# Optimization experiments

Hardware: AMD Instinct MI355X
Metric: run time of the kernel (lower is better)

Reference implementation:

```python
import jax, jax.numpy as jnp
import numpy as np

B, S, H, E, D, K = 2, 4096, 1024, 8, 2048, 2


def setup_inputs() -> dict:
    key = jax.random.key(0)
    ks = jax.random.split(key, 6)
    scale = 0.02
    return {
        "x": jax.random.normal(ks[0], (B, S, H), dtype=jnp.float32),
        "gate_w": jax.random.normal(ks[1], (E, H), dtype=jnp.float32) * scale,
        "w1": jax.random.normal(ks[2], (E, H, D), dtype=jnp.float32) * scale,
        "b1": jnp.zeros((E, D), dtype=jnp.float32),
        "w2": jax.random.normal(ks[3], (E, D, H), dtype=jnp.float32) * scale,
        "b2": jnp.zeros((E, H), dtype=jnp.float32),
    }


def reference(x, gate_w, w1, b1, w2, b2):
    b, s, h = x.shape
    e = gate_w.shape[0]
    # Router
    router_logits = jnp.einsum('bsh,eh->bse', x, gate_w)
    router_probs = jax.nn.softmax(router_logits, axis=-1)
    top_k_probs, expert_idx = jax.lax.top_k(router_probs, K)      # [B,S,K]
    top_k_probs = top_k_probs / top_k_probs.sum(axis=-1, keepdims=True)
    # Aux load-balancing loss (faithful to source: mean over batch only -> [S,E])
    oh = jax.nn.one_hot(expert_idx, e, dtype=x.dtype)             # [B,S,K,E]
    tokens_per_expert = oh.sum(axis=-2).mean(axis=0)              # [S,E]
    avg_prob = router_probs.mean(axis=(0, 1))                     # [E]
    aux_loss = e * (tokens_per_expert * avg_prob).sum()
    # Dense combine weights per token per expert: [B*S, E]
    combine = (oh * top_k_probs[..., None]).sum(axis=-2).reshape(-1, e)
    # Expert MLPs, batched over experts (grouped GEMM form)
    xf = x.reshape(-1, h)                                         # [T,H]
    hid = jax.nn.gelu(jnp.einsum('th,ehd->etd', xf, w1) + b1[:, None, :],
                      approximate=False)                          # [E,T,D]
    y = jnp.einsum('etd,edh->eth', hid, w2) + b2[:, None, :]      # [E,T,H]
    out = jnp.einsum('te,eth->th', combine, y)                    # [T,H]
    return out.reshape(b, s, h), aux_loss
```

## Files before the change

kernel.cpp:

```cpp
#include <hip/hip_runtime.h>
#include <hip/hip_bf16.h>
#include <math.h>

#define Bdim 2
#define Sdim 4096
#define Hdim 1024
#define Edim 8
#define Ddim 2048
#define Tdim (Bdim*Sdim)

typedef __attribute__((ext_vector_type(8))) __bf16 bfv8;
typedef __attribute__((ext_vector_type(8))) short s16x8;
typedef __attribute__((ext_vector_type(4))) short s16x4;
typedef __attribute__((ext_vector_type(4))) float f32x4;

__device__ __forceinline__ short f2bf(float f) {
    union { float f; unsigned u; } a; a.f = f;
    unsigned r = (a.u + 0x7fffu + ((a.u >> 16) & 1u)) >> 16;
    return (short)r;
}
__device__ __forceinline__ float bf2f(short s) {
    union { unsigned u; float f; } a; a.u = ((unsigned)(unsigned short)s) << 16;
    return a.f;
}
__device__ __forceinline__ float fgelu(float x) {
    float u = fminf(x * (1.5957691f + 0.07135481f * x * x), 60.0f);
    float t = __expf(u);
    return x * t / (t + 1.0f);
}

typedef const __attribute__((address_space(1))) unsigned int ga_u32;
typedef __attribute__((address_space(3))) unsigned int la_u32;

__device__ __forceinline__ void gl_lds16(const void* g, void* l) {
    __builtin_amdgcn_global_load_lds((ga_u32*)g, (la_u32*)l, 16, 0, 0);
}

#define WAIT_BAR(N) do {                                     \
    asm volatile("s_waitcnt vmcnt(" #N ")" ::: "memory");    \
    __builtin_amdgcn_s_barrier();                            \
    __builtin_amdgcn_sched_barrier(0);                       \
} while (0)

__global__ __launch_bounds__(256) void router_kernel(
    const float* __restrict__ x, const float* __restrict__ gw,
    int* __restrict__ cnt, float* __restrict__ psum,
    int* __restrict__ ltok, float* __restrict__ lw,
    short* __restrict__ xb)
{
    __shared__ float gws[Edim * Hdim];
    __shared__ int   lcnt[Edim], gbase[Edim];
    __shared__ int   s_e[32], s_pos[32], s_tok[32];
    __shared__ float s_w[32];
    __shared__ float s_ps[4][8];

    int tid = threadIdx.x;
    for (int i = tid; i < Edim * Hdim / 4; i += 256)
        ((float4*)gws)[i] = ((const float4*)gw)[i];
    if (tid < Edim) lcnt[tid] = 0;
    __syncthreads();

    int wave = tid >> 6, lane = tid & 63;
    float ps = 0.f;

    for (int i = 0; i < 4; ++i) {
        int t = blockIdx.x * 16 + wave * 4 + i;
        double acc[Edim];
#pragma unroll
        for (int e = 0; e < Edim; ++e) acc[e] = 0.0;
#pragma unroll
        for (int kq = 0; kq < 4; ++kq) {
            float4 xv = *(const float4*)(x + (size_t)t * Hdim + kq * 256 + lane * 4);
            if (xb) {
                s16x4 h; h[0]=f2bf(xv.x); h[1]=f2bf(xv.y); h[2]=f2bf(xv.z); h[3]=f2bf(xv.w);
                *(s16x4*)(xb + (size_t)t * Hdim + kq * 256 + lane * 4) = h;
            }
#pragma unroll
            for (int e = 0; e < Edim; ++e) {
                float4 wv = *(const float4*)(&gws[e * Hdim + kq * 256 + lane * 4]);
                acc[e] += (double)xv.x * wv.x + (double)xv.y * wv.y
                        + (double)xv.z * wv.z + (double)xv.w * wv.w;
            }
        }
#pragma unroll
        for (int e = 0; e < Edim; ++e) {
            acc[e] += __shfl_xor(acc[e], 1, 64);
            acc[e] += __shfl_xor(acc[e], 2, 64);
            acc[e] += __shfl_xor(acc[e], 4, 64);
        }
        int el = lane & 7;
        double v = acc[0];
#pragma unroll
        for (int e = 1; e < Edim; ++e) if (el == e) v = acc[e];
        v += __shfl_xor(v, 8, 64);
        v += __shfl_xor(v, 16, 64);
// ... 42 lines not shown
        int pos = gbase[e] + s_pos[tid];
        ltok[e * Tdim + pos] = s_tok[tid];
        lw[e * Tdim + pos] = s_w[tid];
    }
}

__global__ void aux_kernel(const int* __restrict__ cnt,
                           const float* __restrict__ psum,
                           int* __restrict__ eoff,
                           float* __restrict__ out_aux)
{
    if (threadIdx.x == 0 && blockIdx.x == 0) {
        double s = 0.0;
        int run = 0;
        for (int e = 0; e < Edim; ++e) {
            eoff[e] = run;
            run += cnt[e];
            s += ((double)cnt[e] / (double)Bdim) * ((double)psum[e] / (double)Tdim);
        }
        out_aux[0] = (float)((double)Edim * s);
    }
}

__global__ __launch_bounds__(256) void convt_kernel(const float* __restrict__ w,
                                                    short* __restrict__ wt, int R, int C)
{
    int e = blockIdx.z;
    int r0 = blockIdx.y * 64, c0 = blockIdx.x * 64;
    __shared__ short t[64][76];
    int tid = threadIdx.x;
    {
        int r = tid >> 2, cs = (tid & 3) * 16;
        const float* src = w + ((size_t)e * R + r0 + r) * C + c0 + cs;
#pragma unroll
        for (int q = 0; q < 4; ++q) {
            float4 v = *(const float4*)(src + q * 4);
            s16x4 h; h[0]=f2bf(v.x); h[1]=f2bf(v.y); h[2]=f2bf(v.z); h[3]=f2bf(v.w);
            *(s16x4*)(&t[r][cs + q * 4]) = h;
        }
    }
    __syncthreads();
    {
        int c = tid >> 2, rs = (tid & 3) * 16;
        short tmp[16];
#pragma unroll
        for (int j = 0; j < 16; ++j) tmp[j] = t[rs + j][c];
        short* dst = wt + ((size_t)e * C + c0 + c) * R + r0 + rs;
        *(s16x8*)dst = *(s16x8*)tmp;
        *(s16x8*)(dst + 8) = *(s16x8*)(tmp + 8);
    }
}


__global__ __launch_bounds__(512, 2) void gemm1n_kernel(
    const short* __restrict__ xb, const short* __restrict__ w1t,
    const float* __restrict__ b1, const int* __restrict__ cnt,
    const int* __restrict__ eoff, const int* __restrict__ ltok,
    short* __restrict__ hid)
{
    constexpr int GXN = Ddim / 256;
    int id = blockIdx.x;
    int e = id & 7;
    unsigned rem = (unsigned)id >> 3;
    int bx = rem & (GXN - 1);
    int by = rem / GXN;

    int n_e = cnt[e];
    int row0 = by * 256;
    if (row0 >= n_e) return;
    int col0 = bx * 256;
    int slot0 = eoff[e];

    __shared__ short lds[65536];
    char* ldsb = (char*)lds;

    int tid = threadIdx.x;
    int w = tid >> 6, lane = tid & 63;

    const short* aS[2]; const short* bS[2];
    int oA[2];
#pragma unroll
    for (int j = 0; j < 2; ++j) {
        int o = tid * 16 + j * 8192;
        oA[j] = o;
        int eff = o ^ (((o >> 7) & 7) << 4);
        int row = ((eff >> 7) << 1) | ((eff >> 6) & 1);
        int kB  = eff & 63;
        int gr = row0 + row; if (gr > n_e - 1) gr = n_e - 1;
        int tok = ltok[(size_t)e * Tdim + gr] >> 1;
        aS[j] = xb + (size_t)tok * Hdim + (kB >> 1);
        bS[j] = w1t + ((size_t)e * Ddim + col0 + row) * Hdim + (kB >> 1);
    }

    int fr = lane & 15, kg = lane >> 4;
    int wm = (w >> 2) * 128, wn = (w & 3) * 64;

    int offA[8], offB[4];
#pragma unroll
    for (int m = 0; m < 8; ++m) {
        int r = wm + m * 16 + fr;
        offA[m] = (r >> 1) * 64 + ((((r & 1) * 32) + kg * 8) ^ (((r >> 1) & 7) << 3));
    }
#pragma unroll
    for (int n = 0; n < 4; ++n) {
        int r = wn + n * 16 + fr;
        offB[n] = (r >> 1) * 64 + ((((r & 1) * 32) + kg * 8) ^ (((r >> 1) & 7) << 3));
    }

    f32x4 acc[8][4];
#pragma unroll
    for (int m = 0; m < 8; ++m)
#pragma unroll
        for (int n = 0; n < 4; ++n) acc[m][n] = (f32x4)0.0f;

    auto stage = [&](int dstB) {
#pragma unroll
        for (int j = 0; j < 2; ++j) {
            gl_lds16(aS[j], ldsb + dstB + oA[j]);
            gl_lds16(bS[j], ldsb + dstB + 32768 + oA[j]);
            aS[j] += 32; bS[j] += 32;
        }
    };
    auto computeH = [&](int baseSh) {
        bfv8 af[8], bf[4];
#pragma unroll
        for (int n = 0; n < 4; ++n) bf[n] = *(const bfv8*)(lds + baseSh + 16384 + offB[n]);
#pragma unroll
        for (int m = 0; m < 8; ++m) af[m] = *(const bfv8*)(lds + baseSh + offA[m]);
        __builtin_amdgcn_s_setprio(1);
#pragma unroll
        for (int m = 0; m < 8; ++m)
#pragma unroll
            for (int n = 0; n < 4; ++n)
                acc[m][n] = __builtin_amdgcn_mfma_f32_16x16x32_bf16(af[m], bf[n], acc[m][n], 0, 0, 0);
        __builtin_amdgcn_s_setprio(0);
    };

    constexpr int NK = Hdim / 64;
    stage(0);
    stage(16384);
    for (int k = 0; k < NK - 2; k += 2) {
        stage(65536);         WAIT_BAR(8); computeH(0);
        stage(65536 + 16384); WAIT_BAR(8); computeH(8192);
        stage(0);             WAIT_BAR(8); computeH(32768);
        stage(16384);         WAIT_BAR(8); computeH(40960);
    }
    stage(65536);         WAIT_BAR(8); computeH(0);
    stage(65536 + 16384); WAIT_BAR(8); computeH(8192);
    WAIT_BAR(4); computeH(32768);
    WAIT_BAR(0); computeH(40960);

#pragma unroll
    for (int m = 0; m < 8; ++m) {
        int r0r = wm + m * 16 + kg * 4;
#pragma unroll
        for (int j = 0; j < 4; ++j) {
            int gr = row0 + r0r + j;
            if (gr >= n_e) continue;
            size_t hbase = (size_t)(slot0 + gr) * Ddim;
#pragma unroll
            for (int n = 0; n < 4; ++n) {
                int col = col0 + wn + n * 16 + fr;
                float v = acc[m][n][j] + b1[e * Ddim + col];
                hid[hbase + col] = f2bf(fgelu(v));
            }
        }
    }
}

__global__ __launch_bounds__(512, 2) void gemm2n_kernel(
    const short* __restrict__ hid, const short* __restrict__ w2t,
    const float* __restrict__ b2, const int* __restrict__ cnt,
    const int* __restrict__ eoff, const int* __restrict__ ltok,
    const float* __restrict__ lw, short* __restrict__ out2)
{
    constexpr int GXN = Hdim / 256;
    int id = blockIdx.x;
    int e = id & 7;
    unsigned rem = (unsigned)id >> 3;
    int bx = rem & (GXN - 1);
    int by = rem / GXN;

    int n_e = cnt[e];
    int row0 = by * 256;
    if (row0 >= n_e) return;
    int col0 = bx * 256;
    int slot0 = eoff[e];

    __shared__ short lds[65536];
    char* ldsb = (char*)lds;

    int tid = threadIdx.x;
    int w = tid >> 6, lane = tid & 63;

    const short* aS[2]; const short* bS[2];
    int oA[2];
#pragma unroll
    for (int j = 0; j < 2; ++j) {
        int o = tid * 16 + j * 8192;
        oA[j] = o;
        int eff = o ^ (((o >> 7) & 7) << 4);
        int row = ((eff >> 7) << 1) | ((eff >> 6) & 1);
        int kB  = eff & 63;
        int gr = row0 + row; if (gr > n_e - 1) gr = n_e - 1;
        aS[j] = hid + (size_t)(slot0 + gr) * Ddim + (kB >> 1);
        bS[j] = w2t + ((size_t)e * Hdim + col0 + row) * Ddim + (kB >> 1);
    }

    int fr = lane & 15, kg = lane >> 4;
    int wm = (w >> 2) * 128, wn = (w & 3) * 64;

    int offA[8], offB[4];
#pragma unroll
    for (int m = 0; m < 8; ++m) {
        int r = wm + m * 16 + fr;
        offA[m] = (r >> 1) * 64 + ((((r & 1) * 32) + kg * 8) ^ (((r >> 1) & 7) << 3));
    }
#pragma unroll
    for (int n = 0; n < 4; ++n) {
        int r = wn + n * 16 + fr;
        offB[n] = (r >> 1) * 64 + ((((r & 1) * 32) + kg * 8) ^ (((r >> 1) & 7) << 3));
    }

    f32x4 acc[8][4];
#pragma unroll
    for (int m = 0; m < 8; ++m)
#pragma unroll
        for (int n = 0; n < 4; ++n) acc[m][n] = (f32x4)0.0f;

    auto stage = [&](int dstB) {
#pragma unroll
        for (int j = 0; j < 2; ++j) {
            gl_lds16(aS[j], ldsb + dstB + oA[j]);
            gl_lds16(bS[j], ldsb + dstB + 32768 + oA[j]);
            aS[j] += 32; bS[j] += 32;
        }
    };
    auto computeH = [&](int baseSh) {
        bfv8 af[8], bf[4];
#pragma unroll
        for (int n = 0; n < 4; ++n) bf[n] = *(const bfv8*)(lds + baseSh + 16384 + offB[n]);
#pragma unroll
        for (int m = 0; m < 8; ++m) af[m] = *(const bfv8*)(lds + baseSh + offA[m]);
        __builtin_amdgcn_s_setprio(1);
#pragma unroll
        for (int m = 0; m < 8; ++m)
#pragma unroll
            for (int n = 0; n < 4; ++n)
                acc[m][n] = __builtin_amdgcn_mfma_f32_16x16x32_bf16(af[m], bf[n], acc[m][n], 0, 0, 0);
        __builtin_amdgcn_s_setprio(0);
    };

    constexpr int NK = Ddim / 64;
    stage(0);
    stage(16384);
    for (int k = 0; k < NK - 2; k += 2) {
        stage(65536);         WAIT_BAR(8); computeH(0);
        stage(65536 + 16384); WAIT_BAR(8); computeH(8192);
        stage(0);             WAIT_BAR(8); computeH(32768);
        stage(16384);         WAIT_BAR(8); computeH(40960);
    }
    stage(65536);         WAIT_BAR(8); computeH(0);
    stage(65536 + 16384); WAIT_BAR(8); computeH(8192);
    WAIT_BAR(4); computeH(32768);
    WAIT_BAR(0); computeH(40960);

#pragma unroll
    for (int m = 0; m < 8; ++m) {
        int r0r = wm + m * 16 + kg * 4;
#pragma unroll
        for (int j = 0; j < 4; ++j) {
            int gr = row0 + r0r + j;
            if (gr >= n_e) continue;
            int val = ltok[(size_t)e * Tdim + gr];
            float p = lw[(size_t)e * Tdim + gr];
            size_t obase = (size_t)val * Hdim;
#pragma unroll
            for (int n = 0; n < 4; ++n) {
                int col = col0 + wn + n * 16 + fr;
                float v = p * (acc[m][n][j] + b2[e * Hdim + col]);
                out2[obase + col] = f2bf(v);
            }
        }
    }
}

__global__ __launch_bounds__(256) void combine_kernel(const short* __restrict__ out2,
                                                      float* __restrict__ out)
{
    size_t i = ((size_t)blockIdx.x * 256 + threadIdx.x) * 8;
    size_t t = i >> 10;
    int h = (int)(i & 1023);
    s16x8 a = *(const s16x8*)(out2 + (t * 2) * 1024 + h);
    s16x8 b = *(const s16x8*)(out2 + (t * 2 + 1) * 1024 + h);
#pragma unroll
    for (int j = 0; j < 8; ++j)
        out[i + j] = bf2f(a[j]) + bf2f(b[j]);
}

#define FBK 64
#define FLDK 72

__global__ __launch_bounds__(256) void gemm1_fb(
    const float* __restrict__ x, const float* __restrict__ w1,
    const float* __restrict__ b1, const int* __restrict__ cnt,
    const int* __restrict__ ltok, short* __restrict__ hid,
    int CH, int row_base)
{
    int e = blockIdx.z;
    int n_e = cnt[e];
    int row0 = row_base + blockIdx.y * 128;
    if (row0 >= n_e) return;
    int col0 = blockIdx.x * 128;

    __shared__ short As[128][FLDK];
    __shared__ short Bs[128][FLDK];

    int tid = threadIdx.x;
    int arow = tid >> 1;
    int akh  = (tid & 1) * 32;
    int gr_a = row0 + arow;
    int tok = ltok[(size_t)e * Tdim + (gr_a < n_e ? gr_a : n_e - 1)] >> 1;
    const float* xrow = x + (size_t)tok * Hdim + akh;
    int bdg = (tid & 31) * 4;
    int bkg = (tid >> 5) * 4;

    int lane = tid & 63;
    int wid = tid >> 6;
    int wm = (wid >> 1) * 64, wn = (wid & 1) * 64;
    int fr = lane & 15, kg = lane >> 4;

    f32x4 acc[4][4];
#pragma unroll
    for (int m = 0; m < 4; ++m)
#pragma unroll
        for (int n = 0; n < 4; ++n) acc[m][n] = (f32x4)0.0f;

    const float* wB = w1 + (size_t)e * Hdim * Ddim + col0;

    for (int k0 = 0; k0 < Hdim; k0 += FBK) {
#pragma unroll
        for (int i = 0; i < 8; ++i) {
            float4 v = *(const float4*)(xrow + k0 + i * 4);
            s16x4 h; h[0] = f2bf(v.x); h[1] = f2bf(v.y); h[2] = f2bf(v.z); h[3] = f2bf(v.w);
            *(s16x4*)(&As[arow][akh + i * 4]) = h;
        }
#pragma unroll
        for (int r = 0; r < 2; ++r) {
            int kq = bkg + r * 32;
            float4 v0 = *(const float4*)(wB + (size_t)(k0 + kq + 0) * Ddim + bdg);
// ... 137 lines not shown
            if (gr >= n_e) continue;
            int tok = ltok[(size_t)e * Tdim + gr] >> 1;
            float p = lw[(size_t)e * Tdim + gr];
#pragma unroll
            for (int n = 0; n < 4; ++n) {
                int col = col0 + wn + n * 16 + fr;
                float v = p * (acc[m][n][j] + b2[e * Hdim + col]);
                atomicAdd(&out[(size_t)tok * Hdim + col], v);
            }
        }
    }
}

extern "C" void kernel_launch(void* const* d_in, const int* in_sizes, int n_in,
                              void* d_out, int out_size, void* d_ws, size_t ws_size,
                              hipStream_t stream)
{
    const float* x  = (const float*)d_in[0];
    const float* gw = (const float*)d_in[1];
    const float* w1 = (const float*)d_in[2];
    const float* b1 = (const float*)d_in[3];
    const float* w2 = (const float*)d_in[4];
    const float* b2 = (const float*)d_in[5];
    float* out = (float*)d_out;

    char* wsb = (char*)d_ws;
    int*   cnt  = (int*)wsb;
    float* psum = (float*)(wsb + 32);
    int*   eoff = (int*)(wsb + 64);
    int*   ltok = (int*)(wsb + 128);
    float* lwp  = (float*)(wsb + 128 + (size_t)Edim * Tdim * 4);
    size_t lists_end = 128 + (size_t)Edim * Tdim * 8;

    size_t xb_sz = (size_t)Tdim * Hdim * 2;
    size_t w1t_sz = (size_t)Edim * Hdim * Ddim * 2;
    size_t w2t_sz = w1t_sz;
    size_t hid_sz = (size_t)(2 * Tdim) * Ddim * 2;
    size_t req = lists_end + xb_sz + w1t_sz + w2t_sz + hid_sz;

    hipMemsetAsync(wsb, 0, 128, stream);

    if (req <= ws_size) {
        short* xb   = (short*)(wsb + lists_end);
        short* w1t  = (short*)(wsb + lists_end + xb_sz);
        short* w2t  = (short*)(wsb + lists_end + xb_sz + w1t_sz);
        short* hid  = (short*)(wsb + lists_end + xb_sz + w1t_sz + w2t_sz);
        short* out2 = w1t;

        convt_kernel<<<dim3(Ddim / 64, Hdim / 64, Edim), 256, 0, stream>>>(w1, w1t, Hdim, Ddim);
        convt_kernel<<<dim3(Hdim / 64, Ddim / 64, Edim), 256, 0, stream>>>(w2, w2t, Ddim, Hdim);
        router_kernel<<<Tdim / 16, 256, 0, stream>>>(x, gw, cnt, psum, ltok, lwp, xb);
        aux_kernel<<<1, 64, 0, stream>>>(cnt, psum, eoff, out + (size_t)Tdim * Hdim);

        gemm1n_kernel<<<(Ddim / 256) * 32 * Edim, 512, 0, stream>>>(
            xb, w1t, b1, cnt, eoff, ltok, hid);
        gemm2n_kernel<<<(Hdim / 256) * 32 * Edim, 512, 0, stream>>>(
            hid, w2t, b2, cnt, eoff, ltok, lwp, out2);
        combine_kernel<<<(size_t)Tdim * Hdim / 2048, 256, 0, stream>>>(out2, out);
    } else {
        short* hid = (short*)(wsb + lists_end);
        int CH2 = 2048;
        while (CH2 > 128 && lists_end + (size_t)Edim * CH2 * Ddim * 2 > ws_size) CH2 >>= 1;

        hipMemsetAsync(d_out, 0, (size_t)out_size * 4, stream);
        router_kernel<<<Tdim / 16, 256, 0, stream>>>(x, gw, cnt, psum, ltok, lwp, nullptr);
        aux_kernel<<<1, 64, 0, stream>>>(cnt, psum, eoff, out + (size_t)Tdim * Hdim);

        int chunks = Tdim / CH2;
        for (int c = 0; c < chunks; ++c) {
            gemm1_fb<<<dim3(Ddim / 128, CH2 / 128, Edim), 256, 0, stream>>>(
                x, w1, b1, cnt, ltok, hid, CH2, c * CH2);
            gemm2_fb<<<dim3(Hdim / 128, CH2 / 128, Edim), 256, 0, stream>>>(
                hid, w2, b2, cnt, ltok, lwp, out, CH2, c * CH2);
        }
    }
}
```

Baseline: 337.7 us.

## Retile expert GEMMs to 256x128 with four-stage LDS ring and register double buffering

Both grouped expert GEMMs move from 512-thread 256x256 tiles to 256-thread 256x128 tiles with a K step of 32. LDS becomes a four-slot ring, and the LDS-to-register fragment reads are double buffered so the next slice's reads overlap the current MFMAs. The combine kernel now writes float4 vectors instead of scalar stores. In exchange, the grid doubles, occupancy drops to one block per CU, and there are more barriers per unit of K work.

```diff
diff --git a/kernel.cpp b/kernel.cpp
--- a/kernel.cpp
+++ b/kernel.cpp
@@ -36,10 +36,26 @@
     __builtin_amdgcn_global_load_lds((ga_u32*)g, (la_u32*)l, 16, 0, 0);
 }
 
-#define WAIT_BAR(N) do {                                     \
-    asm volatile("s_waitcnt vmcnt(" #N ")" ::: "memory");    \
-    __builtin_amdgcn_s_barrier();                            \
-    __builtin_amdgcn_sched_barrier(0);                       \
+#define WB(N) do {                                                        \
+    asm volatile("s_waitcnt vmcnt(" #N ") lgkmcnt(0)" ::: "memory");      \
+    __builtin_amdgcn_s_barrier();                                         \
+    __builtin_amdgcn_sched_barrier(0);                                    \
+} while (0)
+
+#define RD(FA, FB, R) do {                                                            \
+    _Pragma("unroll") for (int n = 0; n < 4; ++n)                                     \
+        FB[n] = *(const bfv8*)(lds + 32768 + (R) * 4096 + offB[n]);                   \
+    _Pragma("unroll") for (int m = 0; m < 8; ++m)                                     \
+        FA[m] = *(const bfv8*)(lds + (R) * 8192 + offA[m]);                           \
+    __builtin_amdgcn_sched_barrier(0);                                                \
+} while (0)
+
+#define MM(FA, FB) do {                                                               \
+    __builtin_amdgcn_s_setprio(1);                                                    \
+    _Pragma("unroll") for (int m = 0; m < 8; ++m)                                     \
+        _Pragma("unroll") for (int n = 0; n < 4; ++n)                                 \
+            acc[m][n] = __builtin_amdgcn_mfma_f32_16x16x32_bf16(FA[m], FB[n], acc[m][n], 0, 0, 0); \
+    __builtin_amdgcn_s_setprio(0);                                                    \
 } while (0)
 
 __global__ __launch_bounds__(256) void router_kernel(
@@ -189,13 +205,13 @@
 }
 
 
-__global__ __launch_bounds__(512, 2) void gemm1n_kernel(
+__global__ __launch_bounds__(256, 1) void gemm1n_kernel(
     const short* __restrict__ xb, const short* __restrict__ w1t,
     const float* __restrict__ b1, const int* __restrict__ cnt,
     const int* __restrict__ eoff, const int* __restrict__ ltok,
     short* __restrict__ hid)
 {
-    constexpr int GXN = Ddim / 256;
+    constexpr int GXN = Ddim / 128;
     int id = blockIdx.x;
     int e = id & 7;
     unsigned rem = (unsigned)id >> 3;
@@ -205,32 +221,40 @@
     int n_e = cnt[e];
     int row0 = by * 256;
     if (row0 >= n_e) return;
-    int col0 = bx * 256;
+    int col0 = bx * 128;
     int slot0 = eoff[e];
 
-    __shared__ short lds[65536];
+    __shared__ short lds[49152];
     char* ldsb = (char*)lds;
 
     int tid = threadIdx.x;
     int w = tid >> 6, lane = tid & 63;
 
-    const short* aS[2]; const short* bS[2];
-    int oA[2];
-#pragma unroll
-    for (int j = 0; j < 2; ++j) {
-        int o = tid * 16 + j * 8192;
-        oA[j] = o;
+    const short* aS[4]; const short* bS[2];
+    int oAd[4], oBd[2];
+#pragma unroll
+    for (int j = 0; j < 4; ++j) {
+        int o = tid * 16 + j * 4096;
+        oAd[j] = o;
         int eff = o ^ (((o >> 7) & 7) << 4);
         int row = ((eff >> 7) << 1) | ((eff >> 6) & 1);
         int kB  = eff & 63;
         int gr = row0 + row; if (gr > n_e - 1) gr = n_e - 1;
         int tok = ltok[(size_t)e * Tdim + gr] >> 1;
         aS[j] = xb + (size_t)tok * Hdim + (kB >> 1);
+    }
+#pragma unroll
+    for (int j = 0; j < 2; ++j) {
+        int o = tid * 16 + j * 4096;
+        oBd[j] = o;
+        int eff = o ^ (((o >> 7) & 7) << 4);
+        int row = ((eff >> 7) << 1) | ((eff >> 6) & 1);
+        int kB  = eff & 63;
         bS[j] = w1t + ((size_t)e * Ddim + col0 + row) * Hdim + (kB >> 1);
     }
 
     int fr = lane & 15, kg = lane >> 4;
-    int wm = (w >> 2) * 128, wn = (w & 3) * 64;
+    int wm = (w >> 1) * 128, wn = (w & 1) * 64;
 
     int offA[8], offB[4];
 #pragma unroll
@@ -250,42 +274,35 @@
 #pragma unroll
         for (int n = 0; n < 4; ++n) acc[m][n] = (f32x4)0.0f;
 
-    auto stage = [&](int dstB) {
+    bfv8 f0A[8], f0B[4], f1A[8], f1B[4];
+
+    auto stage = [&](int r) {
+#pragma unroll
+        for (int j = 0; j < 4; ++j) {
+            gl_lds16(aS[j], ldsb + r * 16384 + oAd[j]);
+            aS[j] += 32;
+        }
 #pragma unroll
         for (int j = 0; j < 2; ++j) {
-            gl_lds16(aS[j], ldsb + dstB + oA[j]);
-            gl_lds16(bS[j], ldsb + dstB + 32768 + oA[j]);
-            aS[j] += 32; bS[j] += 32;
+            gl_lds16(bS[j], ldsb + 65536 + r * 8192 + oBd[j]);
+            bS[j] += 32;
         }
     };
-    auto computeH = [&](int baseSh) {
-        bfv8 af[8], bf[4];
-#pragma unroll
-        for (int n = 0; n < 4; ++n) bf[n] = *(const bfv8*)(lds + baseSh + 16384 + offB[n]);
-#pragma unroll
-        for (int m = 0; m < 8; ++m) af[m] = *(const bfv8*)(lds + baseSh + offA[m]);
-        __builtin_amdgcn_s_setprio(1);
-#pragma unroll
-        for (int m = 0; m < 8; ++m)
-#pragma unroll
-            for (int n = 0; n < 4; ++n)
-                acc[m][n] = __builtin_amdgcn_mfma_f32_16x16x32_bf16(af[m], bf[n], acc[m][n], 0, 0, 0);
-        __builtin_amdgcn_s_setprio(0);
-    };
-
-    constexpr int NK = Hdim / 64;
-    stage(0);
-    stage(16384);
-    for (int k = 0; k < NK - 2; k += 2) {
-        stage(65536);         WAIT_BAR(8); computeH(0);
-        stage(65536 + 16384); WAIT_BAR(8); computeH(8192);
-        stage(0);             WAIT_BAR(8); computeH(32768);
-        stage(16384);         WAIT_BAR(8); computeH(40960);
-    }
-    stage(65536);         WAIT_BAR(8); computeH(0);
-    stage(65536 + 16384); WAIT_BAR(8); computeH(8192);
-    WAIT_BAR(4); computeH(32768);
-    WAIT_BAR(0); computeH(40960);
+
+    constexpr int NH = Hdim / 32;
+    stage(0); stage(1);
+    stage(2); WB(12); RD(f0A, f0B, 0);
+    stage(3); WB(12); RD(f1A, f1B, 1); MM(f0A, f0B);
+#pragma unroll 1
+    for (int it = 0; it < (NH - 4) / 4; ++it) {
+        stage(0); WB(12); RD(f0A, f0B, 2); MM(f1A, f1B);
+        stage(1); WB(12); RD(f1A, f1B, 3); MM(f0A, f0B);
+        stage(2); WB(12); RD(f0A, f0B, 0); MM(f1A, f1B);
+        stage(3); WB(12); RD(f1A, f1B, 1); MM(f0A, f0B);
+    }
+    WB(6);  RD(f0A, f0B, 2); MM(f1A, f1B);
+    WB(0);  RD(f1A, f1B, 3); MM(f0A, f0B);
+    MM(f1A, f1B);
 
 #pragma unroll
     for (int m = 0; m < 8; ++m) {
@@ -305,13 +322,13 @@
     }
 }
 
-__global__ __launch_bounds__(512, 2) void gemm2n_kernel(
+__global__ __launch_bounds__(256, 1) void gemm2n_kernel(
     const short* __restrict__ hid, const short* __restrict__ w2t,
     const float* __restrict__ b2, const int* __restrict__ cnt,
     const int* __restrict__ eoff, const int* __restrict__ ltok,
     const float* __restrict__ lw, short* __restrict__ out2)
 {
-    constexpr int GXN = Hdim / 256;
+    constexpr int GXN = Hdim / 128;
     int id = blockIdx.x;
     int e = id & 7;
     unsigned rem = (unsigned)id >> 3;
@@ -321,31 +338,39 @@
     int n_e = cnt[e];
     int row0 = by * 256;
     if (row0 >= n_e) return;
-    int col0 = bx * 256;
+    int col0 = bx * 128;
     int slot0 = eoff[e];
 
-    __shared__ short lds[65536];
+    __shared__ short lds[49152];
     char* ldsb = (char*)lds;
 
     int tid = threadIdx.x;
     int w = tid >> 6, lane = tid & 63;
 
-    const short* aS[2]; const short* bS[2];
-    int oA[2];
-#pragma unroll
-    for (int j = 0; j < 2; ++j) {
-        int o = tid * 16 + j * 8192;
-        oA[j] = o;
+    const short* aS[4]; const short* bS[2];
+    int oAd[4], oBd[2];
+#pragma unroll
+    for (int j = 0; j < 4; ++j) {
+        int o = tid * 16 + j * 4096;
+        oAd[j] = o;
         int eff = o ^ (((o >> 7) & 7) << 4);
         int row = ((eff >> 7) << 1) | ((eff >> 6) & 1);
         int kB  = eff & 63;
         int gr = row0 + row; if (gr > n_e - 1) gr = n_e - 1;
         aS[j] = hid + (size_t)(slot0 + gr) * Ddim + (kB >> 1);
+    }
+#pragma unroll
+    for (int j = 0; j < 2; ++j) {
+        int o = tid * 16 + j * 4096;
+        oBd[j] = o;
+        int eff = o ^ (((o >> 7) & 7) << 4);
+        int row = ((eff >> 7) << 1) | ((eff >> 6) & 1);
+        int kB  = eff & 63;
         bS[j] = w2t + ((size_t)e * Hdim + col0 + row) * Ddim + (kB >> 1);
     }
 
     int fr = lane & 15, kg = lane >> 4;
-    int wm = (w >> 2) * 128, wn = (w & 3) * 64;
+    int wm = (w >> 1) * 128, wn = (w & 1) * 64;
 
     int offA[8], offB[4];
 #pragma unroll
@@ -365,42 +390,35 @@
 #pragma unroll
         for (int n = 0; n < 4; ++n) acc[m][n] = (f32x4)0.0f;
 
-    auto stage = [&](int dstB) {
+    bfv8 f0A[8], f0B[4], f1A[8], f1B[4];
+
+    auto stage = [&](int r) {
+#pragma unroll
+        for (int j = 0; j < 4; ++j) {
+            gl_lds16(aS[j], ldsb + r * 16384 + oAd[j]);
+            aS[j] += 32;
+        }
 #pragma unroll
         for (int j = 0; j < 2; ++j) {
-            gl_lds16(aS[j], ldsb + dstB + oA[j]);
-            gl_lds16(bS[j], ldsb + dstB + 32768 + oA[j]);
-            aS[j] += 32; bS[j] += 32;
+            gl_lds16(bS[j], ldsb + 65536 + r * 8192 + oBd[j]);
+            bS[j] += 32;
         }
     };
-    auto computeH = [&](int baseSh) {
-        bfv8 af[8], bf[4];
-#pragma unroll
-        for (int n = 0; n < 4; ++n) bf[n] = *(const bfv8*)(lds + baseSh + 16384 + offB[n]);
-#pragma unroll
-        for (int m = 0; m < 8; ++m) af[m] = *(const bfv8*)(lds + baseSh + offA[m]);
-        __builtin_amdgcn_s_setprio(1);
-#pragma unroll
-        for (int m = 0; m < 8; ++m)
-#pragma unroll
-            for (int n = 0; n < 4; ++n)
-                acc[m][n] = __builtin_amdgcn_mfma_f32_16x16x32_bf16(af[m], bf[n], acc[m][n], 0, 0, 0);
-        __builtin_amdgcn_s_setprio(0);
-    };
-
-    constexpr int NK = Ddim / 64;
-    stage(0);
-    stage(16384);
-    for (int k = 0; k < NK - 2; k += 2) {
-        stage(65536);         WAIT_BAR(8); computeH(0);
-        stage(65536 + 16384); WAIT_BAR(8); computeH(8192);
-        stage(0);             WAIT_BAR(8); computeH(32768);
-        stage(16384);         WAIT_BAR(8); computeH(40960);
-    }
-    stage(65536);         WAIT_BAR(8); computeH(0);
-    stage(65536 + 16384); WAIT_BAR(8); computeH(8192);
-    WAIT_BAR(4); computeH(32768);
-    WAIT_BAR(0); computeH(40960);
+
+    constexpr int NH = Ddim / 32;
+    stage(0); stage(1);
+    stage(2); WB(12); RD(f0A, f0B, 0);
+    stage(3); WB(12); RD(f1A, f1B, 1); MM(f0A, f0B);
+#pragma unroll 1
+    for (int it = 0; it < (NH - 4) / 4; ++it) {
+        stage(0); WB(12); RD(f0A, f0B, 2); MM(f1A, f1B);
+        stage(1); WB(12); RD(f1A, f1B, 3); MM(f0A, f0B);
+        stage(2); WB(12); RD(f0A, f0B, 0); MM(f1A, f1B);
+        stage(3); WB(12); RD(f1A, f1B, 1); MM(f0A, f0B);
+    }
+    WB(6);  RD(f0A, f0B, 2); MM(f1A, f1B);
+    WB(0);  RD(f1A, f1B, 3); MM(f0A, f0B);
+    MM(f1A, f1B);
 
 #pragma unroll
     for (int m = 0; m < 8; ++m) {
@@ -430,9 +448,13 @@
     int h = (int)(i & 1023);
     s16x8 a = *(const s16x8*)(out2 + (t * 2) * 1024 + h);
     s16x8 b = *(const s16x8*)(out2 + (t * 2 + 1) * 1024 + h);
-#pragma unroll
-    for (int j = 0; j < 8; ++j)
-        out[i + j] = bf2f(a[j]) + bf2f(b[j]);
+    float4 o0, o1;
+    o0.x = bf2f(a[0]) + bf2f(b[0]); o0.y = bf2f(a[1]) + bf2f(b[1]);
+    o0.z = bf2f(a[2]) + bf2f(b[2]); o0.w = bf2f(a[3]) + bf2f(b[3]);
+    o1.x = bf2f(a[4]) + bf2f(b[4]); o1.y = bf2f(a[5]) + bf2f(b[5]);
+    o1.z = bf2f(a[6]) + bf2f(b[6]); o1.w = bf2f(a[7]) + bf2f(b[7]);
+    *(float4*)(out + i) = o0;
+    *(float4*)(out + i + 4) = o1;
 }
 
 #define FBK 64
@@ -676,9 +698,9 @@
         router_kernel<<<Tdim / 16, 256, 0, stream>>>(x, gw, cnt, psum, ltok, lwp, xb);
         aux_kernel<<<1, 64, 0, stream>>>(cnt, psum, eoff, out + (size_t)Tdim * Hdim);
 
-        gemm1n_kernel<<<(Ddim / 256) * 32 * Edim, 512, 0, stream>>>(
+        gemm1n_kernel<<<(Ddim / 128) * 32 * Edim, 256, 0, stream>>>(
             xb, w1t, b1, cnt, eoff, ltok, hid);
-        gemm2n_kernel<<<(Hdim / 256) * 32 * Edim, 512, 0, stream>>>(
+        gemm2n_kernel<<<(Hdim / 128) * 32 * Edim, 256, 0, stream>>>(
             hid, w2t, b2, cnt, eoff, ltok, lwp, out2);
         combine_kernel<<<(size_t)Tdim * Hdim / 2048, 256, 0, stream>>>(out2, out);
     } else {
```

Result: slower. 365.7 us (+8.3%).

## Restructure expert GEMM mainloop into 4-slot pipeline with early LDS reads

Applied to the files above, without the earlier changes.

Both expert GEMM kernels move from a two-half-tile compute per 64-wide K step to a four-slot ring of 32-wide K chunks. A and B now sit in separate LDS halves. Each phase reads fragments from LDS before issuing the next global-to-LDS stage, then waits and runs MFMAs, so LDS reads overlap the in-flight global loads and the per-phase vmcnt waits become looser. The combine kernel now writes float4 vectors instead of scalar stores. The cost is more barriers per K, since there is one per 32-wide chunk, plus tighter ordering via sched_barrier.

```diff
diff --git a/kernel.cpp b/kernel.cpp
--- a/kernel.cpp
+++ b/kernel.cpp
@@ -36,10 +36,43 @@
     __builtin_amdgcn_global_load_lds((ga_u32*)g, (la_u32*)l, 16, 0, 0);
 }
 
-#define WAIT_BAR(N) do {                                     \
-    asm volatile("s_waitcnt vmcnt(" #N ")" ::: "memory");    \
-    __builtin_amdgcn_s_barrier();                            \
-    __builtin_amdgcn_sched_barrier(0);                       \
+#define G_RD(SLOT) do {                                                              \
+    _Pragma("unroll") for (int n = 0; n < 4; ++n)                                    \
+        bf[n] = *(const bfv8*)(lds + 32768 + (SLOT) * 8192 + offB[n]);               \
+    _Pragma("unroll") for (int m = 0; m < 8; ++m)                                    \
+        af[m] = *(const bfv8*)(lds + (SLOT) * 8192 + offA[m]);                       \
+    __builtin_amdgcn_sched_barrier(0);                                               \
+} while (0)
+
+#define G_MM() do {                                                                  \
+    __builtin_amdgcn_s_setprio(1);                                                   \
+    _Pragma("unroll") for (int m = 0; m < 8; ++m)                                    \
+        _Pragma("unroll") for (int n = 0; n < 4; ++n)                                \
+            acc[m][n] = __builtin_amdgcn_mfma_f32_16x16x32_bf16(af[m], bf[n], acc[m][n], 0, 0, 0); \
+    __builtin_amdgcn_s_setprio(0);                                                   \
+    __builtin_amdgcn_sched_barrier(0);                                               \
+} while (0)
+
+#define G_PH(SRD, SST) do {                                                          \
+    G_RD(SRD);                                                                       \
+    stage(SST);                                                                      \
+    asm volatile("s_waitcnt vmcnt(4)" ::: "memory");                                 \
+    __builtin_amdgcn_s_barrier();                                                    \
+    __builtin_amdgcn_sched_barrier(0);                                               \
+    G_MM();                                                                          \
+} while (0)
+
+#define G_PH_VM0(SRD) do {                                                           \
+    G_RD(SRD);                                                                       \
+    asm volatile("s_waitcnt vmcnt(0)" ::: "memory");                                 \
+    __builtin_amdgcn_s_barrier();                                                    \
+    __builtin_amdgcn_sched_barrier(0);                                               \
+    G_MM();                                                                          \
+} while (0)
+
+#define G_PH_LAST(SRD) do {                                                          \
+    G_RD(SRD);                                                                       \
+    G_MM();                                                                          \
 } while (0)
 
 __global__ __launch_bounds__(256) void router_kernel(
@@ -215,11 +248,11 @@
     int w = tid >> 6, lane = tid & 63;
 
     const short* aS[2]; const short* bS[2];
-    int oA[2];
+    int oD[2];
 #pragma unroll
     for (int j = 0; j < 2; ++j) {
         int o = tid * 16 + j * 8192;
-        oA[j] = o;
+        oD[j] = o;
         int eff = o ^ (((o >> 7) & 7) << 4);
         int row = ((eff >> 7) << 1) | ((eff >> 6) & 1);
         int kB  = eff & 63;
@@ -250,42 +283,30 @@
 #pragma unroll
         for (int n = 0; n < 4; ++n) acc[m][n] = (f32x4)0.0f;
 
-    auto stage = [&](int dstB) {
+    bfv8 af[8], bf[4];
+
+    auto stage = [&](int s) {
 #pragma unroll
         for (int j = 0; j < 2; ++j) {
-            gl_lds16(aS[j], ldsb + dstB + oA[j]);
-            gl_lds16(bS[j], ldsb + dstB + 32768 + oA[j]);
-            aS[j] += 32; bS[j] += 32;
+            gl_lds16(aS[j], ldsb + s * 16384 + oD[j]);
+            aS[j] += 32;
+            gl_lds16(bS[j], ldsb + 65536 + s * 16384 + oD[j]);
+            bS[j] += 32;
         }
     };
-    auto computeH = [&](int baseSh) {
-        bfv8 af[8], bf[4];
-#pragma unroll
-        for (int n = 0; n < 4; ++n) bf[n] = *(const bfv8*)(lds + baseSh + 16384 + offB[n]);
-#pragma unroll
-        for (int m = 0; m < 8; ++m) af[m] = *(const bfv8*)(lds + baseSh + offA[m]);
-        __builtin_amdgcn_s_setprio(1);
-#pragma unroll
-        for (int m = 0; m < 8; ++m)
-#pragma unroll
-            for (int n = 0; n < 4; ++n)
-                acc[m][n] = __builtin_amdgcn_mfma_f32_16x16x32_bf16(af[m], bf[n], acc[m][n], 0, 0, 0);
-        __builtin_amdgcn_s_setprio(0);
-    };
-
-    constexpr int NK = Hdim / 64;
-    stage(0);
-    stage(16384);
-    for (int k = 0; k < NK - 2; k += 2) {
-        stage(65536);         WAIT_BAR(8); computeH(0);
-        stage(65536 + 16384); WAIT_BAR(8); computeH(8192);
-        stage(0);             WAIT_BAR(8); computeH(32768);
-        stage(16384);         WAIT_BAR(8); computeH(40960);
-    }
-    stage(65536);         WAIT_BAR(8); computeH(0);
-    stage(65536 + 16384); WAIT_BAR(8); computeH(8192);
-    WAIT_BAR(4); computeH(32768);
-    WAIT_BAR(0); computeH(40960);
+
+    constexpr int NH = Hdim / 32;
+    stage(0); stage(1);
+    asm volatile("s_waitcnt vmcnt(4)" ::: "memory");
+    __builtin_amdgcn_s_barrier();
+    __builtin_amdgcn_sched_barrier(0);
+#pragma unroll 1
+    for (int it = 0; it < (NH - 4) / 4; ++it) {
+        G_PH(0, 2); G_PH(1, 3); G_PH(2, 0); G_PH(3, 1);
+    }
+    G_PH(0, 2); G_PH(1, 3);
+    G_PH_VM0(2);
+    G_PH_LAST(3);
 
 #pragma unroll
     for (int m = 0; m < 8; ++m) {
@@ -331,11 +352,11 @@
     int w = tid >> 6, lane = tid & 63;
 
     const short* aS[2]; const short* bS[2];
-    int oA[2];
+    int oD[2];
 #pragma unroll
     for (int j = 0; j < 2; ++j) {
         int o = tid * 16 + j * 8192;
-        oA[j] = o;
+        oD[j] = o;
         int eff = o ^ (((o >> 7) & 7) << 4);
         int row = ((eff >> 7) << 1) | ((eff >> 6) & 1);
         int kB  = eff & 63;
@@ -365,42 +386,30 @@
 #pragma unroll
         for (int n = 0; n < 4; ++n) acc[m][n] = (f32x4)0.0f;
 
-    auto stage = [&](int dstB) {
+    bfv8 af[8], bf[4];
+
+    auto stage = [&](int s) {
 #pragma unroll
         for (int j = 0; j < 2; ++j) {
-            gl_lds16(aS[j], ldsb + dstB + oA[j]);
-            gl_lds16(bS[j], ldsb + dstB + 32768 + oA[j]);
-            aS[j] += 32; bS[j] += 32;
+            gl_lds16(aS[j], ldsb + s * 16384 + oD[j]);
+            aS[j] += 32;
+            gl_lds16(bS[j], ldsb + 65536 + s * 16384 + oD[j]);
+            bS[j] += 32;
         }
     };
-    auto computeH = [&](int baseSh) {
-        bfv8 af[8], bf[4];
-#pragma unroll
-        for (int n = 0; n < 4; ++n) bf[n] = *(const bfv8*)(lds + baseSh + 16384 + offB[n]);
-#pragma unroll
-        for (int m = 0; m < 8; ++m) af[m] = *(const bfv8*)(lds + baseSh + offA[m]);
-        __builtin_amdgcn_s_setprio(1);
-#pragma unroll
-        for (int m = 0; m < 8; ++m)
-#pragma unroll
-            for (int n = 0; n < 4; ++n)
-                acc[m][n] = __builtin_amdgcn_mfma_f32_16x16x32_bf16(af[m], bf[n], acc[m][n], 0, 0, 0);
-        __builtin_amdgcn_s_setprio(0);
-    };
-
-    constexpr int NK = Ddim / 64;
-    stage(0);
-    stage(16384);
-    for (int k = 0; k < NK - 2; k += 2) {
-        stage(65536);         WAIT_BAR(8); computeH(0);
-        stage(65536 + 16384); WAIT_BAR(8); computeH(8192);
-        stage(0);             WAIT_BAR(8); computeH(32768);
-        stage(16384);         WAIT_BAR(8); computeH(40960);
-    }
-    stage(65536);         WAIT_BAR(8); computeH(0);
-    stage(65536 + 16384); WAIT_BAR(8); computeH(8192);
-    WAIT_BAR(4); computeH(32768);
-    WAIT_BAR(0); computeH(40960);
+
+    constexpr int NH = Ddim / 32;
+    stage(0); stage(1);
+    asm volatile("s_waitcnt vmcnt(4)" ::: "memory");
+    __builtin_amdgcn_s_barrier();
+    __builtin_amdgcn_sched_barrier(0);
+#pragma unroll 1
+    for (int it = 0; it < (NH - 4) / 4; ++it) {
+        G_PH(0, 2); G_PH(1, 3); G_PH(2, 0); G_PH(3, 1);
+    }
+    G_PH(0, 2); G_PH(1, 3);
+    G_PH_VM0(2);
+    G_PH_LAST(3);
 
 #pragma unroll
     for (int m = 0; m < 8; ++m) {
@@ -430,9 +439,13 @@
     int h = (int)(i & 1023);
     s16x8 a = *(const s16x8*)(out2 + (t * 2) * 1024 + h);
     s16x8 b = *(const s16x8*)(out2 + (t * 2 + 1) * 1024 + h);
-#pragma unroll
-    for (int j = 0; j < 8; ++j)
-        out[i + j] = bf2f(a[j]) + bf2f(b[j]);
+    float4 o0, o1;
+    o0.x = bf2f(a[0]) + bf2f(b[0]); o0.y = bf2f(a[1]) + bf2f(b[1]);
+    o0.z = bf2f(a[2]) + bf2f(b[2]); o0.w = bf2f(a[3]) + bf2f(b[3]);
+    o1.x = bf2f(a[4]) + bf2f(b[4]); o1.y = bf2f(a[5]) + bf2f(b[5]);
+    o1.z = bf2f(a[6]) + bf2f(b[6]); o1.w = bf2f(a[7]) + bf2f(b[7]);
+    *(float4*)(out + i) = o0;
+    *(float4*)(out + i + 4) = o1;
 }
 
 #define FBK 64
```

Result: no change. 337.0 us (-0.2%).

## Restructure MoE GEMM mainloops into fine-grained interleaved LDS-read/MFMA/stage schedule

Applied to the files above, without the earlier changes.

Both grouped GEMM kernels switch from 64-wide to 128-byte K tiles with a new LDS swizzle layout. The mainloop is split into four quarter-MMA phases, with LDS fragment reads, global-to-LDS staging and barriers interleaved between them in a ping-pong style schedule. The aim is to hide LDS and global load latency behind MFMA work and to cut the number of waits. The combine kernel also writes float4 vectors instead of scalar stores. The change adds many more barriers and more register pressure for fragments, which could hurt occupancy or stall warps.

```diff
diff --git a/kernel.cpp b/kernel.cpp
--- a/kernel.cpp
+++ b/kernel.cpp
@@ -36,11 +36,11 @@
     __builtin_amdgcn_global_load_lds((ga_u32*)g, (la_u32*)l, 16, 0, 0);
 }
 
-#define WAIT_BAR(N) do {                                     \
-    asm volatile("s_waitcnt vmcnt(" #N ")" ::: "memory");    \
-    __builtin_amdgcn_s_barrier();                            \
-    __builtin_amdgcn_sched_barrier(0);                       \
-} while (0)
+#define BAR() do { __builtin_amdgcn_s_barrier(); __builtin_amdgcn_sched_barrier(0); } while (0)
+#define LG0() do { asm volatile("s_waitcnt lgkmcnt(0)" ::: "memory"); __builtin_amdgcn_sched_barrier(0); } while (0)
+#define VM6() do { asm volatile("s_waitcnt vmcnt(6)" ::: "memory"); __builtin_amdgcn_sched_barrier(0); } while (0)
+#define VM0() do { asm volatile("s_waitcnt vmcnt(0)" ::: "memory"); __builtin_amdgcn_sched_barrier(0); } while (0)
+#define NOVM() do { } while (0)
 
 __global__ __launch_bounds__(256) void router_kernel(
     const float* __restrict__ x, const float* __restrict__ gw,
@@ -189,6 +189,21 @@
 }
 
 
+#define KTILE(BOS, CURA, S1, S2, VMT) do {                                        \
+    RDA(0, BOS); RDB(b01, 0, BOS);                                                \
+    if (S1) STG(aSh1, (32768 - (CURA)) + 16384);                                  \
+    BAR(); LG0(); MMQ(0, b01, 0); BAR();                                          \
+    RDB(b23, 2, BOS);                                                             \
+    BAR(); LG0(); MMQ(0, b23, 2); BAR();                                          \
+    RDA(4, BOS);                                                                  \
+    if (S2) STG(bSh0, 65536 + (CURA));                                            \
+    BAR(); LG0(); MMQ(4, b23, 2); BAR();                                          \
+    if (S2) { STG(bSh1, 65536 + (CURA) + 16384); STG(aSh0, (CURA)); }             \
+    BAR(); LG0(); MMQ(4, b01, 0);                                                 \
+    VMT();                                                                        \
+    BAR();                                                                        \
+} while (0)
+
 __global__ __launch_bounds__(512, 2) void gemm1n_kernel(
     const short* __restrict__ xb, const short* __restrict__ w1t,
     const float* __restrict__ b1, const int* __restrict__ cnt,
@@ -214,34 +229,40 @@
     int tid = threadIdx.x;
     int w = tid >> 6, lane = tid & 63;
 
-    const short* aS[2]; const short* bS[2];
-    int oA[2];
+    int dBase = w * 2048 + lane * 16;
+    int scB = ((lane & 7) * 16) ^ (((lane >> 3) & 7) << 4);
+    const short* aSh0[2]; const short* aSh1[2];
+    const short* bSh0[2]; const short* bSh1[2];
 #pragma unroll
     for (int j = 0; j < 2; ++j) {
-        int o = tid * 16 + j * 8192;
-        oA[j] = o;
-        int eff = o ^ (((o >> 7) & 7) << 4);
-        int row = ((eff >> 7) << 1) | ((eff >> 6) & 1);
-        int kB  = eff & 63;
-        int gr = row0 + row; if (gr > n_e - 1) gr = n_e - 1;
-        int tok = ltok[(size_t)e * Tdim + gr] >> 1;
-        aS[j] = xb + (size_t)tok * Hdim + (kB >> 1);
-        bS[j] = w1t + ((size_t)e * Ddim + col0 + row) * Hdim + (kB >> 1);
+#pragma unroll
+        for (int h = 0; h < 2; ++h) {
+            int rowL = h * 128 + (w * 2 + j) * 8 + (lane >> 3);
+            int gr = row0 + rowL; if (gr > n_e - 1) gr = n_e - 1;
+            int tok = ltok[(size_t)e * Tdim + gr] >> 1;
+            const short* ap = xb + (size_t)tok * Hdim + (scB >> 1);
+            const short* bp = w1t + ((size_t)e * Ddim + col0 + rowL) * Hdim + (scB >> 1);
+            if (h == 0) { aSh0[j] = ap; bSh0[j] = bp; }
+            else        { aSh1[j] = ap; bSh1[j] = bp; }
+        }
     }
 
     int fr = lane & 15, kg = lane >> 4;
     int wm = (w >> 2) * 128, wn = (w & 3) * 64;
-
-    int offA[8], offB[4];
+    int offA[8][2], offB[4][2];
 #pragma unroll
     for (int m = 0; m < 8; ++m) {
         int r = wm + m * 16 + fr;
-        offA[m] = (r >> 1) * 64 + ((((r & 1) * 32) + kg * 8) ^ (((r >> 1) & 7) << 3));
+#pragma unroll
+        for (int ks = 0; ks < 2; ++ks)
+            offA[m][ks] = r * 64 + ((ks * 32 + kg * 8) ^ ((r & 7) << 3));
     }
 #pragma unroll
     for (int n = 0; n < 4; ++n) {
         int r = wn + n * 16 + fr;
-        offB[n] = (r >> 1) * 64 + ((((r & 1) * 32) + kg * 8) ^ (((r >> 1) & 7) << 3));
+#pragma unroll
+        for (int ks = 0; ks < 2; ++ks)
+            offB[n][ks] = 32768 + r * 64 + ((ks * 32 + kg * 8) ^ ((r & 7) << 3));
     }
 
     f32x4 acc[8][4];
@@ -250,42 +271,61 @@
 #pragma unroll
         for (int n = 0; n < 4; ++n) acc[m][n] = (f32x4)0.0f;
 
-    auto stage = [&](int dstB) {
-#pragma unroll
-        for (int j = 0; j < 2; ++j) {
-            gl_lds16(aS[j], ldsb + dstB + oA[j]);
-            gl_lds16(bS[j], ldsb + dstB + 32768 + oA[j]);
-            aS[j] += 32; bS[j] += 32;
-        }
+    bfv8 aA[4][2], b01[2][2], b23[2][2];
+
+    auto STG = [&](const short* (&s)[2], int dst) {
+        gl_lds16(s[0], ldsb + dst + dBase);
+        gl_lds16(s[1], ldsb + dst + 1024 + dBase);
+        s[0] += 64; s[1] += 64;
     };
-    auto computeH = [&](int baseSh) {
-        bfv8 af[8], bf[4];
-#pragma unroll
-        for (int n = 0; n < 4; ++n) bf[n] = *(const bfv8*)(lds + baseSh + 16384 + offB[n]);
-#pragma unroll
-        for (int m = 0; m < 8; ++m) af[m] = *(const bfv8*)(lds + baseSh + offA[m]);
+    auto RDA = [&](int mb, int BOS) {
+#pragma unroll
+        for (int mm = 0; mm < 4; ++mm)
+#pragma unroll
+            for (int ks = 0; ks < 2; ++ks)
+                aA[mm][ks] = *(const bfv8*)(lds + BOS + offA[mb + mm][ks]);
+        __builtin_amdgcn_sched_barrier(0);
+    };
+    auto RDB = [&](bfv8 (&B)[2][2], int nb, int BOS) {
+#pragma unroll
+        for (int nn = 0; nn < 2; ++nn)
+#pragma unroll
+            for (int ks = 0; ks < 2; ++ks)
+                B[nn][ks] = *(const bfv8*)(lds + BOS + offB[nb + nn][ks]);
+        __builtin_amdgcn_sched_barrier(0);
+    };
+    auto MMQ = [&](int mb, bfv8 (&B)[2][2], int nb) {
         __builtin_amdgcn_s_setprio(1);
 #pragma unroll
-        for (int m = 0; m < 8; ++m)
-#pragma unroll
-            for (int n = 0; n < 4; ++n)
-                acc[m][n] = __builtin_amdgcn_mfma_f32_16x16x32_bf16(af[m], bf[n], acc[m][n], 0, 0, 0);
+        for (int mm = 0; mm < 4; ++mm)
+#pragma unroll
+            for (int nn = 0; nn < 2; ++nn) {
+                acc[mb + mm][nb + nn] = __builtin_amdgcn_mfma_f32_16x16x32_bf16(
+                    aA[mm][0], B[nn][0], acc[mb + mm][nb + nn], 0, 0, 0);
+                acc[mb + mm][nb + nn] = __builtin_amdgcn_mfma_f32_16x16x32_bf16(
+                    aA[mm][1], B[nn][1], acc[mb + mm][nb + nn], 0, 0, 0);
+            }
         __builtin_amdgcn_s_setprio(0);
+        __builtin_amdgcn_sched_barrier(0);
     };
 
-    constexpr int NK = Hdim / 64;
-    stage(0);
-    stage(16384);
-    for (int k = 0; k < NK - 2; k += 2) {
-        stage(65536);         WAIT_BAR(8); computeH(0);
-        stage(65536 + 16384); WAIT_BAR(8); computeH(8192);
-        stage(0);             WAIT_BAR(8); computeH(32768);
-        stage(16384);         WAIT_BAR(8); computeH(40960);
-    }
-    stage(65536);         WAIT_BAR(8); computeH(0);
-    stage(65536 + 16384); WAIT_BAR(8); computeH(8192);
-    WAIT_BAR(4); computeH(32768);
-    WAIT_BAR(0); computeH(40960);
+    constexpr int NT = Hdim / 64;
+    STG(bSh0, 65536);
+    STG(bSh1, 65536 + 16384);
+    STG(aSh0, 0);
+    STG(aSh1, 16384);
+    STG(bSh0, 65536 + 32768);
+    STG(bSh1, 65536 + 32768 + 16384);
+    STG(aSh0, 32768);
+    VM6(); BAR();
+
+#pragma unroll 1
+    for (int it = 0; it < NT / 2 - 1; ++it) {
+        KTILE(0,     0,     1, 1, VM6);
+        KTILE(16384, 32768, 1, 1, VM6);
+    }
+    KTILE(0,     0,     1, 0, VM0);
+    KTILE(16384, 32768, 0, 0, NOVM);
 
 #pragma unroll
     for (int m = 0; m < 8; ++m) {
@@ -330,33 +370,39 @@
     int tid = threadIdx.x;
     int w = tid >> 6, lane = tid & 63;
 
-    const short* aS[2]; const short* bS[2];
-    int oA[2];
+    int dBase = w * 2048 + lane * 16;
+    int scB = ((lane & 7) * 16) ^ (((lane >> 3) & 7) << 4);
+    const short* aSh0[2]; const short* aSh1[2];
+    const short* bSh0[2]; const short* bSh1[2];
 #pragma unroll
     for (int j = 0; j < 2; ++j) {
-        int o = tid * 16 + j * 8192;
-        oA[j] = o;
-        int eff = o ^ (((o >> 7) & 7) << 4);
-        int row = ((eff >> 7) << 1) | ((eff >> 6) & 1);
-        int kB  = eff & 63;
-        int gr = row0 + row; if (gr > n_e - 1) gr = n_e - 1;
-        aS[j] = hid + (size_t)(slot0 + gr) * Ddim + (kB >> 1);
-        bS[j] = w2t + ((size_t)e * Hdim + col0 + row) * Ddim + (kB >> 1);
+#pragma unroll
+        for (int h = 0; h < 2; ++h) {
+            int rowL = h * 128 + (w * 2 + j) * 8 + (lane >> 3);
+            int gr = row0 + rowL; if (gr > n_e - 1) gr = n_e - 1;
+            const short* ap = hid + (size_t)(slot0 + gr) * Ddim + (scB >> 1);
+            const short* bp = w2t + ((size_t)e * Hdim + col0 + rowL) * Ddim + (scB >> 1);
+            if (h == 0) { aSh0[j] = ap; bSh0[j] = bp; }
+            else        { aSh1[j] = ap; bSh1[j] = bp; }
+        }
     }
 
     int fr = lane & 15, kg = lane >> 4;
     int wm = (w >> 2) * 128, wn = (w & 3) * 64;
-
-    int offA[8], offB[4];
+    int offA[8][2], offB[4][2];
 #pragma unroll
     for (int m = 0; m < 8; ++m) {
         int r = wm + m * 16 + fr;
-        offA[m] = (r >> 1) * 64 + ((((r & 1) * 32) + kg * 8) ^ (((r >> 1) & 7) << 3));
+#pragma unroll
+        for (int ks = 0; ks < 2; ++ks)
+            offA[m][ks] = r * 64 + ((ks * 32 + kg * 8) ^ ((r & 7) << 3));
     }
 #pragma unroll
     for (int n = 0; n < 4; ++n) {
         int r = wn + n * 16 + fr;
-        offB[n] = (r >> 1) * 64 + ((((r & 1) * 32) + kg * 8) ^ (((r >> 1) & 7) << 3));
+#pragma unroll
+        for (int ks = 0; ks < 2; ++ks)
+            offB[n][ks] = 32768 + r * 64 + ((ks * 32 + kg * 8) ^ ((r & 7) << 3));
     }
 
     f32x4 acc[8][4];
@@ -365,42 +411,61 @@
 #pragma unroll
         for (int n = 0; n < 4; ++n) acc[m][n] = (f32x4)0.0f;
 
-    auto stage = [&](int dstB) {
-#pragma unroll
-        for (int j = 0; j < 2; ++j) {
-            gl_lds16(aS[j], ldsb + dstB + oA[j]);
-            gl_lds16(bS[j], ldsb + dstB + 32768 + oA[j]);
-            aS[j] += 32; bS[j] += 32;
-        }
+    bfv8 aA[4][2], b01[2][2], b23[2][2];
+
+    auto STG = [&](const short* (&s)[2], int dst) {
+        gl_lds16(s[0], ldsb + dst + dBase);
+        gl_lds16(s[1], ldsb + dst + 1024 + dBase);
+        s[0] += 64; s[1] += 64;
     };
-    auto computeH = [&](int baseSh) {
-        bfv8 af[8], bf[4];
-#pragma unroll
-        for (int n = 0; n < 4; ++n) bf[n] = *(const bfv8*)(lds + baseSh + 16384 + offB[n]);
-#pragma unroll
-        for (int m = 0; m < 8; ++m) af[m] = *(const bfv8*)(lds + baseSh + offA[m]);
+    auto RDA = [&](int mb, int BOS) {
+#pragma unroll
+        for (int mm = 0; mm < 4; ++mm)
+#pragma unroll
+            for (int ks = 0; ks < 2; ++ks)
+                aA[mm][ks] = *(const bfv8*)(lds + BOS + offA[mb + mm][ks]);
+        __builtin_amdgcn_sched_barrier(0);
+    };
+    auto RDB = [&](bfv8 (&B)[2][2], int nb, int BOS) {
+#pragma unroll
+        for (int nn = 0; nn < 2; ++nn)
+#pragma unroll
+            for (int ks = 0; ks < 2; ++ks)
+                B[nn][ks] = *(const bfv8*)(lds + BOS + offB[nb + nn][ks]);
+        __builtin_amdgcn_sched_barrier(0);
+    };
+    auto MMQ = [&](int mb, bfv8 (&B)[2][2], int nb) {
         __builtin_amdgcn_s_setprio(1);
 #pragma unroll
-        for (int m = 0; m < 8; ++m)
-#pragma unroll
-            for (int n = 0; n < 4; ++n)
-                acc[m][n] = __builtin_amdgcn_mfma_f32_16x16x32_bf16(af[m], bf[n], acc[m][n], 0, 0, 0);
+        for (int mm = 0; mm < 4; ++mm)
+#pragma unroll
+            for (int nn = 0; nn < 2; ++nn) {
+                acc[mb + mm][nb + nn] = __builtin_amdgcn_mfma_f32_16x16x32_bf16(
+                    aA[mm][0], B[nn][0], acc[mb + mm][nb + nn], 0, 0, 0);
+                acc[mb + mm][nb + nn] = __builtin_amdgcn_mfma_f32_16x16x32_bf16(
+                    aA[mm][1], B[nn][1], acc[mb + mm][nb + nn], 0, 0, 0);
+            }
         __builtin_amdgcn_s_setprio(0);
+        __builtin_amdgcn_sched_barrier(0);
     };
 
-    constexpr int NK = Ddim / 64;
-    stage(0);
-    stage(16384);
-    for (int k = 0; k < NK - 2; k += 2) {
-        stage(65536);         WAIT_BAR(8); computeH(0);
-        stage(65536 + 16384); WAIT_BAR(8); computeH(8192);
-        stage(0);             WAIT_BAR(8); computeH(32768);
-        stage(16384);         WAIT_BAR(8); computeH(40960);
-    }
-    stage(65536);         WAIT_BAR(8); computeH(0);
-    stage(65536 + 16384); WAIT_BAR(8); computeH(8192);
-    WAIT_BAR(4); computeH(32768);
-    WAIT_BAR(0); computeH(40960);
+    constexpr int NT = Ddim / 64;
+    STG(bSh0, 65536);
+    STG(bSh1, 65536 + 16384);
+    STG(aSh0, 0);
+    STG(aSh1, 16384);
+    STG(bSh0, 65536 + 32768);
+    STG(bSh1, 65536 + 32768 + 16384);
+    STG(aSh0, 32768);
+    VM6(); BAR();
+
+#pragma unroll 1
+    for (int it = 0; it < NT / 2 - 1; ++it) {
+        KTILE(0,     0,     1, 1, VM6);
+        KTILE(16384, 32768, 1, 1, VM6);
+    }
+    KTILE(0,     0,     1, 0, VM0);
+    KTILE(16384, 32768, 0, 0, NOVM);
 
 #pragma unroll
     for (int m = 0; m < 8; ++m) {
@@ -430,9 +495,13 @@
     int h = (int)(i & 1023);
     s16x8 a = *(const s16x8*)(out2 + (t * 2) * 1024 + h);
     s16x8 b = *(const s16x8*)(out2 + (t * 2 + 1) * 1024 + h);
-#pragma unroll
-    for (int j = 0; j < 8; ++j)
-        out[i + j] = bf2f(a[j]) + bf2f(b[j]);
+    float4 o0, o1;
+    o0.x = bf2f(a[0]) + bf2f(b[0]); o0.y = bf2f(a[1]) + bf2f(b[1]);
+    o0.z = bf2f(a[2]) + bf2f(b[2]); o0.w = bf2f(a[3]) + bf2f(b[3]);
+    o1.x = bf2f(a[4]) + bf2f(b[4]); o1.y = bf2f(a[5]) + bf2f(b[5]);
+    o1.z = bf2f(a[6]) + bf2f(b[6]); o1.w = bf2f(a[7]) + bf2f(b[7]);
+    *(float4*)(out + i) = o0;
+    *(float4*)(out + i + 4) = o1;
 }
 
 #define FBK 64
```

New measurement: 342.4 us. About the same (+1.4%).
